# Kernel tuning notes

Hardware: AMD Instinct MI355X
Metric: run time of the kernel (lower is better)

## Reference

```python
import jax, jax.numpy as jnp
import numpy as np

VX, VY = 0.2, 0.2
X_OFF = VX / 2 + 0.0      # pc_range x_min = 0
Y_OFF = VY / 2 + (-40.0)  # pc_range y_min = -40
BN_EPS = 1e-3


def setup_inputs() -> dict:
    key = jax.random.key(0)
    k1, k2, k3, k4, k5, k6 = jax.random.split(key, 6)
    K, P, C_IN, C_AUG, C_OUT = 20000, 100, 4, 9, 64
    features = jax.random.normal(k1, (K, P, C_IN), dtype=jnp.float32)
    # at least 1 point per pillar (avoids div-by-zero, as in real voxelization)
    num_voxels = jax.random.randint(k2, (K,), 1, P + 1, dtype=jnp.int64)
    coors = jax.random.randint(k3, (K, 4), 0, 352, dtype=jnp.int64)
    W = jax.random.normal(k4, (C_AUG, C_OUT), dtype=jnp.float32) * (1.0 / np.sqrt(C_AUG))
    gamma = jnp.ones((C_OUT,), dtype=jnp.float32) + 0.1 * jax.random.normal(k5, (C_OUT,), dtype=jnp.float32)
    beta = 0.1 * jax.random.normal(k6, (C_OUT,), dtype=jnp.float32)
    return {"features": features, "num_voxels": num_voxels, "coors": coors,
            "W": W, "gamma": gamma, "beta": beta}


def reference(features, num_voxels, coors, W, gamma, beta):
    K, P, _ = features.shape
    dt = features.dtype
    pn = num_voxels.astype(dt)[:, None, None]                      # [K,1,1]
    cx = coors[:, 3].astype(dt)[:, None] * VX + X_OFF              # [K,1]
    cy = coors[:, 2].astype(dt)[:, None] * VY + Y_OFF              # [K,1]
    mask = (jnp.arange(P)[None, :] < num_voxels[:, None]).astype(dt)[..., None]  # [K,P,1]
    # cluster offset: point xyz minus per-pillar mean
    points_mean = features[..., :3].sum(axis=-2, keepdims=True) / pn
    f_cluster = features[..., :3] - points_mean                    # [K,P,3]
    # center offset: point xy minus pillar center
    f_center = jnp.stack([features[..., 0] - cx, features[..., 1] - cy], axis=-1)  # [K,P,2]
    feats = jnp.concatenate([features, f_cluster, f_center], axis=-1) * mask       # [K,P,9]
    # PFNLayer: Linear(no bias) -> BatchNorm1d (training-mode batch stats) -> ReLU -> max over points
    x = jnp.einsum('kpc,cu->kpu', feats, W)                        # [K,P,64]
    mu = x.mean(axis=(0, 1))
    var = ((x - mu) ** 2).mean(axis=(0, 1))
    x = (x - mu) * jax.lax.rsqrt(var + BN_EPS) * gamma + beta
    x = jax.nn.relu(x)
    return x.max(axis=1)                                           # [K,64] (squeezed)
```

## Files before the change

kernel.cpp:

```cpp
#include <hip/hip_runtime.h>


typedef float f32x2 __attribute__((ext_vector_type(2)));

#define NQ 14
#define NO 54
#define NP 68

__device__ __forceinline__ float wred(float v) {
#pragma unroll
  for (int off = 1; off < 64; off <<= 1) v += __shfl_xor(v, off, 64);
  return v;
}

__global__ void __launch_bounds__(512) pfn_main(
    const float4* __restrict__ feat, const int* __restrict__ nvox,
    const int* __restrict__ coors, const float* __restrict__ W, int K, int P,
    int nwaves, int nblocks, float* __restrict__ partials,
    float4* __restrict__ ext) {
  __shared__ float4 pts[8][102];
  __shared__ float redQ[8][NQ];
  __shared__ float redO[8][NO];
  const int lane = threadIdx.x & 63;
  const int wid = threadIdx.x >> 6;
  const int hl = lane & 31;
  const int p0 = lane >> 5;

  int c_i = lane, c2_i = lane;
  if (lane >= 9 && lane < NO) {
    int r = lane - 9, c = 0;
    while (r >= 9 - c) { r -= 9 - c; ++c; }
    c_i = c; c2_i = c + r;
  }
  const int gc = (c_i < 4) ? c_i : (c_i < 7 ? c_i - 4 : c_i - 7);
  const int gc2 = (c2_i < 4) ? c2_i : (c2_i < 7 ? c2_i - 4 : c2_i - 7);

  const f32x2* W2 = (const f32x2*)W;
  const f32x2 w4 = W2[4 * 32 + hl], w5 = W2[5 * 32 + hl];
  const f32x2 w6 = W2[6 * 32 + hl], w7 = W2[7 * 32 + hl];
  const f32x2 w8 = W2[8 * 32 + hl];
  const f32x2 wx = W2[0 * 32 + hl] + w4 + w7;
  const f32x2 wy = W2[1 * 32 + hl] + w5 + w8;
  const f32x2 wz = W2[2 * 32 + hl] + w6;
  const f32x2 w3 = W2[3 * 32 + hl];

  float gvx = 0, gvy = 0, gvz = 0, gvw = 0;
  float qxx = 0, qxy = 0, qxz = 0, qxw = 0, qyy = 0;
  float qyz = 0, qyw = 0, qzz = 0, qzw = 0, qww = 0;
  float oacc = 0;

  const int gw = (blockIdx.x * blockDim.x + threadIdx.x) >> 6;
  for (int k = gw; k < K; k += nwaves) {
    const size_t base = (size_t)k * P;
    const int nv = nvox[k];
    float sax = 0, say = 0, saz = 0;
    float svx = 0, svy = 0, svz = 0, svw = 0;
    for (int p = lane; p < P; p += 64) {
      float4 f = feat[base + p];
      pts[wid][p] = f;
      sax += f.x; say += f.y; saz += f.z;
      if (p < nv) {
        svx += f.x; svy += f.y; svz += f.z; svw += f.w;
        qxx = fmaf(f.x, f.x, qxx); qxy = fmaf(f.x, f.y, qxy);
        qxz = fmaf(f.x, f.z, qxz); qxw = fmaf(f.x, f.w, qxw);
        qyy = fmaf(f.y, f.y, qyy); qyz = fmaf(f.y, f.z, qyz);
        qyw = fmaf(f.y, f.w, qyw); qzz = fmaf(f.z, f.z, qzz);
        qzw = fmaf(f.z, f.w, qzw); qww = fmaf(f.w, f.w, qww);
      }
    }
    if ((nv & 1) && nv < P && lane == 0) pts[wid][nv] = pts[wid][0];
    const float rsax = wred(sax), rsay = wred(say), rsaz = wred(saz);
    const float rsvx = wred(svx), rsvy = wred(svy);
    const float rsvz = wred(svz), rsvw = wred(svw);
    gvx += svx; gvy += svy; gvz += svz; gvw += svw;

    const float nvf = (float)nv, inv = 1.f / nvf;
    const float mx = rsax * inv, my = rsay * inv, mz = rsaz * inv;
    const float cx = (float)coors[k * 4 + 3] * 0.2f + 0.1f;
    const float cy = (float)coors[k * 4 + 2] * 0.2f - 39.9f;

    if (lane < 9) {
      const float oc = (lane == 4) ? -mx : (lane == 5) ? -my
                     : (lane == 6) ? -mz : (lane == 7) ? -cx
                     : (lane == 8) ? -cy : 0.f;
      oacc = fmaf(nvf, oc, oacc);
    } else if (lane < NO) {
      const float oc = (c_i == 4) ? -mx : (c_i == 5) ? -my
                     : (c_i == 6) ? -mz : (c_i == 7) ? -cx
                     : (c_i == 8) ? -cy : 0.f;
      const float oc2 = (c2_i == 4) ? -mx : (c2_i == 5) ? -my
                      : (c2_i == 6) ? -mz : (c2_i == 7) ? -cx
                      : (c2_i == 8) ? -cy : 0.f;
      const float sgc = (gc == 0) ? rsvx : (gc == 1) ? rsvy
                      : (gc == 2) ? rsvz : rsvw;
      const float sgc2 = (gc2 == 0) ? rsvx : (gc2 == 1) ? rsvy
                       : (gc2 == 2) ? rsvz : rsvw;
      oacc += oc * sgc2 + oc2 * sgc + nvf * oc * oc2;
    }

    const f32x2 bias = -(mx * w4 + my * w5 + mz * w6 + cx * w7 + cy * w8);
    f32x2 bm0 = {-3e38f, -3e38f}, bm1 = {-3e38f, -3e38f};
    f32x2 bn0 = {3e38f, 3e38f}, bn1 = {3e38f, 3e38f};
    const int nvv = nv + (nv & 1);
    int p = 0;
    for (; p + 4 <= nvv; p += 4) {
      float4 fa = pts[wid][p + p0];
      float4 fb = pts[wid][p + 2 + p0];
      f32x2 ba = wx * fa.x + wy * fa.y + wz * fa.z + w3 * fa.w;
      f32x2 bb = wx * fb.x + wy * fb.y + wz * fb.z + w3 * fb.w;
      bm0.x = fmaxf(bm0.x, ba.x); bm0.y = fmaxf(bm0.y, ba.y);
      bn0.x = fminf(bn0.x, ba.x); bn0.y = fminf(bn0.y, ba.y);
      bm1.x = fmaxf(bm1.x, bb.x); bm1.y = fmaxf(bm1.y, bb.y);
      bn1.x = fminf(bn1.x, bb.x); bn1.y = fminf(bn1.y, bb.y);
    }
    for (; p < nvv; p += 2) {
      float4 fa = pts[wid][p + p0];
      f32x2 ba = wx * fa.x + wy * fa.y + wz * fa.z + w3 * fa.w;
      bm0.x = fmaxf(bm0.x, ba.x); bm0.y = fmaxf(bm0.y, ba.y);
      bn0.x = fminf(bn0.x, ba.x); bn0.y = fminf(bn0.y, ba.y);
    }
    f32x2 bm, bn;
    bm.x = fmaxf(bm0.x, bm1.x); bm.y = fmaxf(bm0.y, bm1.y);
    bn.x = fminf(bn0.x, bn1.x); bn.y = fminf(bn0.y, bn1.y);
    bm.x = fmaxf(bm.x, __shfl_xor(bm.x, 32, 64));
    bm.y = fmaxf(bm.y, __shfl_xor(bm.y, 32, 64));
    bn.x = fminf(bn.x, __shfl_xor(bn.x, 32, 64));
    bn.y = fminf(bn.y, __shfl_xor(bn.y, 32, 64));
    f32x2 vmax = bm + bias, vmin = bn + bias;
    if (nv < P) {
      vmax.x = fmaxf(vmax.x, 0.f); vmax.y = fmaxf(vmax.y, 0.f);
      vmin.x = fminf(vmin.x, 0.f); vmin.y = fminf(vmin.y, 0.f);
    }
    if (lane < 32) {
      float4 e; e.x = vmax.x; e.y = vmax.y; e.z = vmin.x; e.w = vmin.y;
      ext[(size_t)k * 32 + hl] = e;
    }
  }

  float qa[NQ] = {gvx, gvy, gvz, gvw, qxx, qxy, qxz,
                  qxw, qyy, qyz, qyw, qzz, qzw, qww};
#pragma unroll
  for (int i = 0; i < NQ; ++i) qa[i] = wred(qa[i]);
  if (lane == 0) {
#pragma unroll
    for (int i = 0; i < NQ; ++i) redQ[wid][i] = qa[i];
  }
  if (lane < NO) redO[wid][lane] = oacc;
  __syncthreads();
  const int t = threadIdx.x;
  if (t < NQ) {
    float s = 0;
#pragma unroll
    for (int w = 0; w < 8; ++w) s += redQ[w][t];
    partials[t * nblocks + blockIdx.x] = s;
  }
  if (t >= 64 && t < 64 + NO) {
    const int m = t - 64;
    float s = 0;
#pragma unroll
    for (int w = 0; w < 8; ++w) s += redO[w][m];
    partials[(NQ + m) * nblocks + blockIdx.x] = s;
  }
}

__global__ void __launch_bounds__(512) pfn_finalize(
    const float* __restrict__ partials, int nblocks,
    const float* __restrict__ W, const float* __restrict__ gamma,
    const float* __restrict__ beta, float invN, float* __restrict__ ss) {
  __shared__ float msum[NP];
  __shared__ float m54[NO];
  const int t = threadIdx.x;
  const int m = t >> 2, j = t & 3;
  if (m < NP) {
    const int chunk = nblocks >> 2;
    const float* row = partials + m * nblocks + j * chunk;
    float a0 = 0, a1 = 0, a2 = 0, a3 = 0, a4 = 0, a5 = 0, a6 = 0, a7 = 0;
    int b = 0;
    for (; b + 8 <= chunk; b += 8) {
      a0 += row[b];     a1 += row[b + 1]; a2 += row[b + 2]; a3 += row[b + 3];
      a4 += row[b + 4]; a5 += row[b + 5]; a6 += row[b + 6]; a7 += row[b + 7];
    }
    for (; b < chunk; ++b) a0 += row[b];
    float s = ((a0 + a1) + (a2 + a3)) + ((a4 + a5) + (a6 + a7));
    s += __shfl_xor(s, 1, 64);
    s += __shfl_xor(s, 2, 64);
    if (j == 0) msum[m] = s;
  }
  __syncthreads();
  if (t < NO) {
    float v;
    if (t < 9) {
      const int g = (t < 4) ? t : (t < 7 ? t - 4 : t - 7);
      v = msum[g] + msum[NQ + t];
    } else {
      int r = t - 9, c = 0;
      while (r >= 9 - c) { r -= 9 - c; ++c; }
      const int c2 = c + r;
      const int a = (c < 4) ? c : (c < 7 ? c - 4 : c - 7);
      const int b2 = (c2 < 4) ? c2 : (c2 < 7 ? c2 - 4 : c2 - 7);
      const int lo = a < b2 ? a : b2, hi = a < b2 ? b2 : a;
      const int qi = lo * (9 - lo) / 2 + (hi - lo);
      v = msum[4 + qi] + msum[NQ + t];
    }
    m54[t] = v;
  }
  __syncthreads();
  if (t < 64) {
    float wc[9];
#pragma unroll
    for (int c = 0; c < 9; ++c) wc[c] = W[c * 64 + t];
    float mu = 0.f;
#pragma unroll
    for (int c = 0; c < 9; ++c) mu += m54[c] * invN * wc[c];
    float ex2 = 0.f;
    int idx = 9;
#pragma unroll
    for (int c = 0; c < 9; ++c)
#pragma unroll
      for (int c2 = c; c2 < 9; ++c2) {
        float v = m54[idx] * invN * wc[c] * wc[c2];
        ex2 += (c == c2) ? v : 2.f * v;
        ++idx;
      }
    const float var = ex2 - mu * mu;
    const float scale = gamma[t] * rsqrtf(var + 1e-3f);
    ss[t] = scale;
    ss[64 + t] = beta[t] - mu * scale;
  }
}

__global__ void __launch_bounds__(256) pfn_apply(
    const float4* __restrict__ ext, const float* __restrict__ ss, int n,
    f32x2* __restrict__ out) {
  const int t = blockIdx.x * 256 + threadIdx.x;
  if (t >= n) return;
  const int l = t & 31;
  const float4 e = ext[t];
  const f32x2 sc = ((const f32x2*)ss)[l];
  const f32x2 sh = ((const f32x2*)(ss + 64))[l];
  const float v0 = (sc.x >= 0.f) ? e.x : e.z;
  const float v1 = (sc.y >= 0.f) ? e.y : e.w;
  f32x2 o;
  o.x = fmaxf(fmaf(sc.x, v0, sh.x), 0.f);
  o.y = fmaxf(fmaf(sc.y, v1, sh.y), 0.f);
  out[t] = o;
}

extern "C" void kernel_launch(void* const* d_in, const int* in_sizes, int n_in,
                              void* d_out, int out_size, void* d_ws,
                              size_t ws_size, hipStream_t stream) {
  const float4* feat = (const float4*)d_in[0];
  const int* nvox = (const int*)d_in[1];
  const int* coors = (const int*)d_in[2];
  const float* W = (const float*)d_in[3];
  const float* gamma = (const float*)d_in[4];
  const float* beta = (const float*)d_in[5];
  float* out = (float*)d_out;

  const int K = in_sizes[1];
  const int P = in_sizes[0] / (K * 4);

  float* ss = (float*)d_ws;
  float* partials = ss + 128;
  const int nblk = 512;
  float4* ext = (float4*)(partials + NP * nblk);

  pfn_main<<<nblk, 512, 0, stream>>>(feat, nvox, coors, W, K, P, nblk * 8,
                                     nblk, partials, ext);
  pfn_finalize<<<1, 512, 0, stream>>>(partials, nblk, W, gamma, beta,
                                      1.0f / (float)((long long)K * P), ss);
  const int n3 = K * 32;
  pfn_apply<<<(n3 + 255) / 256, 256, 0, stream>>>(ext, ss, n3, (f32x2*)out);
}
```

Before: 46.76 us.

## Prefetch next pillar into double-buffered LDS and restructure moment accumulation

Each wave now handles a contiguous run of pillars instead of striding across the grid. It prefetches the next pillar's features, voxel count and coordinates into registers while computing the current one, and double-buffers the shared-memory point tile. Per-pillar wave reductions of the valid-point sums are removed. Cross terms are instead kept as per-lane outer-product accumulators (S, u1, u2) and reduced once at the end, with the finalize kernel rebuilding the 54 second-moment entries from them. This cuts shuffle work and hides global load latency, at the cost of more registers and a contiguous assignment that may load-balance worse.

New measurement: 53.28 us. 14.0% more time.

```diff
diff --git a/kernel.cpp b/kernel.cpp
--- a/kernel.cpp
+++ b/kernel.cpp
@@ -3,175 +3,211 @@
 
 typedef float f32x2 __attribute__((ext_vector_type(2)));
 
-#define NQ 14
-#define NO 54
-#define NP 68
-
-__device__ __forceinline__ float wred(float v) {
+#define NR 54
+
+__device__ __forceinline__ float wred_add(float v) {
 #pragma unroll
   for (int off = 1; off < 64; off <<= 1) v += __shfl_xor(v, off, 64);
   return v;
+}
+__device__ __forceinline__ f32x2 pmax2(f32x2 a, f32x2 b) {
+  f32x2 r; r.x = fmaxf(a.x, b.x); r.y = fmaxf(a.y, b.y); return r;
+}
+__device__ __forceinline__ f32x2 pmin2(f32x2 a, f32x2 b) {
+  f32x2 r; r.x = fminf(a.x, b.x); r.y = fminf(a.y, b.y); return r;
 }
 
 __global__ void __launch_bounds__(512) pfn_main(
     const float4* __restrict__ feat, const int* __restrict__ nvox,
     const int* __restrict__ coors, const float* __restrict__ W, int K, int P,
-    int nwaves, int nblocks, float* __restrict__ partials,
+    int cnt, int nblocks, float* __restrict__ partials,
     float4* __restrict__ ext) {
-  __shared__ float4 pts[8][102];
-  __shared__ float redQ[8][NQ];
-  __shared__ float redO[8][NO];
+  __shared__ float4 pts[8][2][104];
+  __shared__ float red[8][NR];
   const int lane = threadIdx.x & 63;
   const int wid = threadIdx.x >> 6;
   const int hl = lane & 31;
   const int p0 = lane >> 5;
 
-  int c_i = lane, c2_i = lane;
-  if (lane >= 9 && lane < NO) {
-    int r = lane - 9, c = 0;
-    while (r >= 9 - c) { r -= 9 - c; ++c; }
-    c_i = c; c2_i = c + r;
-  }
-  const int gc = (c_i < 4) ? c_i : (c_i < 7 ? c_i - 4 : c_i - 7);
-  const int gc2 = (c2_i < 4) ? c2_i : (c2_i < 7 ? c2_i - 4 : c2_i - 7);
-
   const f32x2* W2 = (const f32x2*)W;
-  const f32x2 w4 = W2[4 * 32 + hl], w5 = W2[5 * 32 + hl];
-  const f32x2 w6 = W2[6 * 32 + hl], w7 = W2[7 * 32 + hl];
-  const f32x2 w8 = W2[8 * 32 + hl];
-  const f32x2 wx = W2[0 * 32 + hl] + w4 + w7;
-  const f32x2 wy = W2[1 * 32 + hl] + w5 + w8;
-  const f32x2 wz = W2[2 * 32 + hl] + w6;
+  const f32x2 v4 = W2[4 * 32 + hl], v5 = W2[5 * 32 + hl];
+  const f32x2 v6 = W2[6 * 32 + hl], v7 = W2[7 * 32 + hl];
+  const f32x2 v8 = W2[8 * 32 + hl];
+  const f32x2 wx = W2[0 * 32 + hl] + v4 + v7;
+  const f32x2 wy = W2[1 * 32 + hl] + v5 + v8;
+  const f32x2 wz = W2[2 * 32 + hl] + v6;
   const f32x2 w3 = W2[3 * 32 + hl];
 
-  float gvx = 0, gvy = 0, gvz = 0, gvw = 0;
-  float qxx = 0, qxy = 0, qxz = 0, qxw = 0, qyy = 0;
-  float qyz = 0, qyw = 0, qzz = 0, qzw = 0, qww = 0;
-  float oacc = 0;
-
-  const int gw = (blockIdx.x * blockDim.x + threadIdx.x) >> 6;
-  for (int k = gw; k < K; k += nwaves) {
-    const size_t base = (size_t)k * P;
-    const int nv = nvox[k];
-    float sax = 0, say = 0, saz = 0;
-    float svx = 0, svy = 0, svz = 0, svw = 0;
-    for (int p = lane; p < P; p += 64) {
-      float4 f = feat[base + p];
-      pts[wid][p] = f;
-      sax += f.x; say += f.y; saz += f.z;
-      if (p < nv) {
-        svx += f.x; svy += f.y; svz += f.z; svw += f.w;
-        qxx = fmaf(f.x, f.x, qxx); qxy = fmaf(f.x, f.y, qxy);
-        qxz = fmaf(f.x, f.z, qxz); qxw = fmaf(f.x, f.w, qxw);
-        qyy = fmaf(f.y, f.y, qyy); qyz = fmaf(f.y, f.z, qyz);
-        qyw = fmaf(f.y, f.w, qyw); qzz = fmaf(f.z, f.z, qzz);
-        qzw = fmaf(f.z, f.w, qzw); qww = fmaf(f.w, f.w, qww);
-      }
+  float q1[4] = {0, 0, 0, 0};
+  float q2[10] = {0, 0, 0, 0, 0, 0, 0, 0, 0, 0};
+  float S[20];
+  float u1[5] = {0, 0, 0, 0, 0};
+  float u2[15];
+#pragma unroll
+  for (int i = 0; i < 20; ++i) S[i] = 0.f;
+#pragma unroll
+  for (int i = 0; i < 15; ++i) u2[i] = 0.f;
+
+  const int gw = blockIdx.x * 8 + wid;
+  const int k0 = gw * cnt;
+  const int kend = (k0 + cnt < K) ? k0 + cnt : K;
+
+  if (k0 < kend) {
+    const bool hih = (64 + lane) < P;
+    size_t base = (size_t)k0 * P;
+    float4 f0 = feat[base + lane];
+    float4 f1;
+    if (hih) f1 = feat[base + 64 + lane];
+    int nv = nvox[k0];
+    float fcx = (float)coors[k0 * 4 + 3], fcy = (float)coors[k0 * 4 + 2];
+    int cur = 0;
+    for (int k = k0; k < kend; ++k) {
+      pts[wid][cur][lane] = f0;
+      if (hih) pts[wid][cur][64 + lane] = f1;
+      if ((nv & 1) && lane == 0) pts[wid][cur][nv] = f0;
+
+      float sax = f0.x, say = f0.y, saz = f0.z;
+      float svx = 0, svy = 0, svz = 0, svw = 0;
+      if (lane < nv) {
+        svx = f0.x; svy = f0.y; svz = f0.z; svw = f0.w;
+        q2[0] = fmaf(f0.x, f0.x, q2[0]); q2[1] = fmaf(f0.x, f0.y, q2[1]);
+        q2[2] = fmaf(f0.x, f0.z, q2[2]); q2[3] = fmaf(f0.x, f0.w, q2[3]);
+        q2[4] = fmaf(f0.y, f0.y, q2[4]); q2[5] = fmaf(f0.y, f0.z, q2[5]);
+        q2[6] = fmaf(f0.y, f0.w, q2[6]); q2[7] = fmaf(f0.z, f0.z, q2[7]);
+        q2[8] = fmaf(f0.z, f0.w, q2[8]); q2[9] = fmaf(f0.w, f0.w, q2[9]);
+      }
+      if (hih) {
+        sax += f1.x; say += f1.y; saz += f1.z;
+        if (64 + lane < nv) {
+          svx += f1.x; svy += f1.y; svz += f1.z; svw += f1.w;
+          q2[0] = fmaf(f1.x, f1.x, q2[0]); q2[1] = fmaf(f1.x, f1.y, q2[1]);
+          q2[2] = fmaf(f1.x, f1.z, q2[2]); q2[3] = fmaf(f1.x, f1.w, q2[3]);
+          q2[4] = fmaf(f1.y, f1.y, q2[4]); q2[5] = fmaf(f1.y, f1.z, q2[5]);
+          q2[6] = fmaf(f1.y, f1.w, q2[6]); q2[7] = fmaf(f1.z, f1.z, q2[7]);
+          q2[8] = fmaf(f1.z, f1.w, q2[8]); q2[9] = fmaf(f1.w, f1.w, q2[9]);
+        }
+      }
+
+      float4 f0n, f1n;
+      int nvn = nv;
+      float fcxn = fcx, fcyn = fcy;
+      if (k + 1 < kend) {
+        size_t nb = (size_t)(k + 1) * P;
+        f0n = feat[nb + lane];
+        if (hih) f1n = feat[nb + 64 + lane];
+        nvn = nvox[k + 1];
+        fcxn = (float)coors[(k + 1) * 4 + 3];
+        fcyn = (float)coors[(k + 1) * 4 + 2];
+      }
+
+      float rx = sax, ry = say, rz = saz;
+#pragma unroll
+      for (int off = 1; off < 64; off <<= 1) {
+        rx += __shfl_xor(rx, off, 64);
+        ry += __shfl_xor(ry, off, 64);
+        rz += __shfl_xor(rz, off, 64);
+      }
+      const float nvf = (float)nv, inv = 1.f / nvf;
+      const float cx = fcx * 0.2f + 0.1f, cy = fcy * 0.2f - 39.9f;
+      const float o0 = -rx * inv, o1 = -ry * inv, o2 = -rz * inv;
+      const float o3 = -cx, o4 = -cy;
+
+      const int nvv = nv + (nv & 1);
+      f32x2 bm0 = {-3e38f, -3e38f}, bm1 = {-3e38f, -3e38f};
+      f32x2 bn0 = {3e38f, 3e38f}, bn1 = {3e38f, 3e38f};
+      int p = 0;
+      for (; p + 4 <= nvv; p += 4) {
+        float4 fa = pts[wid][cur][p + p0];
+        float4 fb = pts[wid][cur][p + 2 + p0];
+        f32x2 ba = wx * fa.x + wy * fa.y + wz * fa.z + w3 * fa.w;
+        f32x2 bb = wx * fb.x + wy * fb.y + wz * fb.z + w3 * fb.w;
+        bm0 = pmax2(bm0, ba); bn0 = pmin2(bn0, ba);
+        bm1 = pmax2(bm1, bb); bn1 = pmin2(bn1, bb);
+      }
+      if (p < nvv) {
+        float4 fa = pts[wid][cur][p + p0];
+        f32x2 ba = wx * fa.x + wy * fa.y + wz * fa.z + w3 * fa.w;
+        bm0 = pmax2(bm0, ba); bn0 = pmin2(bn0, ba);
+      }
+      f32x2 bm = pmax2(bm0, bm1), bn = pmin2(bn0, bn1);
+      f32x2 tsw;
+      tsw.x = __shfl_xor(bm.x, 32, 64); tsw.y = __shfl_xor(bm.y, 32, 64);
+      bm = pmax2(bm, tsw);
+      tsw.x = __shfl_xor(bn.x, 32, 64); tsw.y = __shfl_xor(bn.y, 32, 64);
+      bn = pmin2(bn, tsw);
+      const f32x2 bias = v4 * o0 + v5 * o1 + v6 * o2 + v7 * o3 + v8 * o4;
+      f32x2 vmax = bm + bias, vmin = bn + bias;
+      if (nv < P) {
+        vmax.x = fmaxf(vmax.x, 0.f); vmax.y = fmaxf(vmax.y, 0.f);
+        vmin.x = fminf(vmin.x, 0.f); vmin.y = fminf(vmin.y, 0.f);
+      }
+      if (lane < 32) {
+        float4 e; e.x = vmax.x; e.y = vmax.y; e.z = vmin.x; e.w = vmin.y;
+        ext[(size_t)k * 32 + hl] = e;
+      }
+
+      q1[0] += svx; q1[1] += svy; q1[2] += svz; q1[3] += svw;
+      const float ov[5] = {o0, o1, o2, o3, o4};
+      const float sv[4] = {svx, svy, svz, svw};
+#pragma unroll
+      for (int a = 0; a < 4; ++a)
+#pragma unroll
+        for (int b = 0; b < 5; ++b)
+          S[a * 5 + b] = fmaf(sv[a], ov[b], S[a * 5 + b]);
+      float no[5];
+#pragma unroll
+      for (int b = 0; b < 5; ++b) { no[b] = nvf * ov[b]; u1[b] += no[b]; }
+      int ui = 0;
+#pragma unroll
+      for (int b = 0; b < 5; ++b)
+#pragma unroll
+        for (int b2 = b; b2 < 5; ++b2) {
+          u2[ui] = fmaf(no[b], ov[b2], u2[ui]);
+          ++ui;
+        }
+
+      f0 = f0n; f1 = f1n; nv = nvn; fcx = fcxn; fcy = fcyn; cur ^= 1;
     }
-    if ((nv & 1) && nv < P && lane == 0) pts[wid][nv] = pts[wid][0];
-    const float rsax = wred(sax), rsay = wred(say), rsaz = wred(saz);
-    const float rsvx = wred(svx), rsvy = wred(svy);
-    const float rsvz = wred(svz), rsvw = wred(svw);
-    gvx += svx; gvy += svy; gvz += svz; gvw += svw;
-
-    const float nvf = (float)nv, inv = 1.f / nvf;
-    const float mx = rsax * inv, my = rsay * inv, mz = rsaz * inv;
-    const float cx = (float)coors[k * 4 + 3] * 0.2f + 0.1f;
-    const float cy = (float)coors[k * 4 + 2] * 0.2f - 39.9f;
-
-    if (lane < 9) {
-      const float oc = (lane == 4) ? -mx : (lane == 5) ? -my
-                     : (lane == 6) ? -mz : (lane == 7) ? -cx
-                     : (lane == 8) ? -cy : 0.f;
-      oacc = fmaf(nvf, oc, oacc);
-    } else if (lane < NO) {
-      const float oc = (c_i == 4) ? -mx : (c_i == 5) ? -my
-                     : (c_i == 6) ? -mz : (c_i == 7) ? -cx
-                     : (c_i == 8) ? -cy : 0.f;
-      const float oc2 = (c2_i == 4) ? -mx : (c2_i == 5) ? -my
-                      : (c2_i == 6) ? -mz : (c2_i == 7) ? -cx
-                      : (c2_i == 8) ? -cy : 0.f;
-      const float sgc = (gc == 0) ? rsvx : (gc == 1) ? rsvy
-                      : (gc == 2) ? rsvz : rsvw;
-      const float sgc2 = (gc2 == 0) ? rsvx : (gc2 == 1) ? rsvy
-                       : (gc2 == 2) ? rsvz : rsvw;
-      oacc += oc * sgc2 + oc2 * sgc + nvf * oc * oc2;
+  }
+
+  {
+    float a34[34];
+#pragma unroll
+    for (int i = 0; i < 4; ++i) a34[i] = q1[i];
+#pragma unroll
+    for (int i = 0; i < 10; ++i) a34[4 + i] = q2[i];
+#pragma unroll
+    for (int i = 0; i < 20; ++i) a34[14 + i] = S[i];
+#pragma unroll
+    for (int i = 0; i < 34; ++i) a34[i] = wred_add(a34[i]);
+    if (lane == 0) {
+#pragma unroll
+      for (int i = 0; i < 34; ++i) red[wid][i] = a34[i];
+#pragma unroll
+      for (int j = 0; j < 5; ++j) red[wid][34 + j] = u1[j];
+#pragma unroll
+      for (int j = 0; j < 15; ++j) red[wid][39 + j] = u2[j];
     }
-
-    const f32x2 bias = -(mx * w4 + my * w5 + mz * w6 + cx * w7 + cy * w8);
-    f32x2 bm0 = {-3e38f, -3e38f}, bm1 = {-3e38f, -3e38f};
-    f32x2 bn0 = {3e38f, 3e38f}, bn1 = {3e38f, 3e38f};
-    const int nvv = nv + (nv & 1);
-    int p = 0;
-    for (; p + 4 <= nvv; p += 4) {
-      float4 fa = pts[wid][p + p0];
-      float4 fb = pts[wid][p + 2 + p0];
-      f32x2 ba = wx * fa.x + wy * fa.y + wz * fa.z + w3 * fa.w;
-      f32x2 bb = wx * fb.x + wy * fb.y + wz * fb.z + w3 * fb.w;
-      bm0.x = fmaxf(bm0.x, ba.x); bm0.y = fmaxf(bm0.y, ba.y);
-      bn0.x = fminf(bn0.x, ba.x); bn0.y = fminf(bn0.y, ba.y);
-      bm1.x = fmaxf(bm1.x, bb.x); bm1.y = fmaxf(bm1.y, bb.y);
-      bn1.x = fminf(bn1.x, bb.x); bn1.y = fminf(bn1.y, bb.y);
-    }
-    for (; p < nvv; p += 2) {
-      float4 fa = pts[wid][p + p0];
-      f32x2 ba = wx * fa.x + wy * fa.y + wz * fa.z + w3 * fa.w;
-      bm0.x = fmaxf(bm0.x, ba.x); bm0.y = fmaxf(bm0.y, ba.y);
-      bn0.x = fminf(bn0.x, ba.x); bn0.y = fminf(bn0.y, ba.y);
-    }
-    f32x2 bm, bn;
-    bm.x = fmaxf(bm0.x, bm1.x); bm.y = fmaxf(bm0.y, bm1.y);
-    bn.x = fminf(bn0.x, bn1.x); bn.y = fminf(bn0.y, bn1.y);
-    bm.x = fmaxf(bm.x, __shfl_xor(bm.x, 32, 64));
-    bm.y = fmaxf(bm.y, __shfl_xor(bm.y, 32, 64));
-    bn.x = fminf(bn.x, __shfl_xor(bn.x, 32, 64));
-    bn.y = fminf(bn.y, __shfl_xor(bn.y, 32, 64));
-    f32x2 vmax = bm + bias, vmin = bn + bias;
-    if (nv < P) {
-      vmax.x = fmaxf(vmax.x, 0.f); vmax.y = fmaxf(vmax.y, 0.f);
-      vmin.x = fminf(vmin.x, 0.f); vmin.y = fminf(vmin.y, 0.f);
-    }
-    if (lane < 32) {
-      float4 e; e.x = vmax.x; e.y = vmax.y; e.z = vmin.x; e.w = vmin.y;
-      ext[(size_t)k * 32 + hl] = e;
-    }
-  }
-
-  float qa[NQ] = {gvx, gvy, gvz, gvw, qxx, qxy, qxz,
-                  qxw, qyy, qyz, qyw, qzz, qzw, qww};
-#pragma unroll
-  for (int i = 0; i < NQ; ++i) qa[i] = wred(qa[i]);
-  if (lane == 0) {
-#pragma unroll
-    for (int i = 0; i < NQ; ++i) redQ[wid][i] = qa[i];
-  }
-  if (lane < NO) redO[wid][lane] = oacc;
+  }
   __syncthreads();
   const int t = threadIdx.x;
-  if (t < NQ) {
-    float s = 0;
-#pragma unroll
-    for (int w = 0; w < 8; ++w) s += redQ[w][t];
+  if (t < NR) {
+    float s = 0.f;
+#pragma unroll
+    for (int w = 0; w < 8; ++w) s += red[w][t];
     partials[t * nblocks + blockIdx.x] = s;
   }
-  if (t >= 64 && t < 64 + NO) {
-    const int m = t - 64;
-    float s = 0;
-#pragma unroll
-    for (int w = 0; w < 8; ++w) s += redO[w][m];
-    partials[(NQ + m) * nblocks + blockIdx.x] = s;
-  }
-}
-
-__global__ void __launch_bounds__(512) pfn_finalize(
+}
+
+__global__ void __launch_bounds__(256) pfn_finalize(
     const float* __restrict__ partials, int nblocks,
     const float* __restrict__ W, const float* __restrict__ gamma,
     const float* __restrict__ beta, float invN, float* __restrict__ ss) {
-  __shared__ float msum[NP];
-  __shared__ float m54[NO];
+  __shared__ float msum[NR];
+  __shared__ float m54[54];
   const int t = threadIdx.x;
   const int m = t >> 2, j = t & 3;
-  if (m < NP) {
+  if (m < NR) {
     const int chunk = nblocks >> 2;
     const float* row = partials + m * nblocks + j * chunk;
     float a0 = 0, a1 = 0, a2 = 0, a3 = 0, a4 = 0, a5 = 0, a6 = 0, a7 = 0;
@@ -187,11 +223,12 @@
     if (j == 0) msum[m] = s;
   }
   __syncthreads();
-  if (t < NO) {
+  if (t < 54) {
     float v;
     if (t < 9) {
       const int g = (t < 4) ? t : (t < 7 ? t - 4 : t - 7);
-      v = msum[g] + msum[NQ + t];
+      v = msum[g];
+      if (t >= 4) v += msum[34 + (t - 4)];
     } else {
       int r = t - 9, c = 0;
       while (r >= 9 - c) { r -= 9 - c; ++c; }
@@ -199,8 +236,13 @@
       const int a = (c < 4) ? c : (c < 7 ? c - 4 : c - 7);
       const int b2 = (c2 < 4) ? c2 : (c2 < 7 ? c2 - 4 : c2 - 7);
       const int lo = a < b2 ? a : b2, hi = a < b2 ? b2 : a;
-      const int qi = lo * (9 - lo) / 2 + (hi - lo);
-      v = msum[4 + qi] + msum[NQ + t];
+      v = msum[4 + lo * (9 - lo) / 2 + (hi - lo)];
+      if (c2 >= 4) v += msum[14 + a * 5 + (c2 - 4)];
+      if (c >= 4) v += msum[14 + b2 * 5 + (c - 4)];
+      if (c >= 4 && c2 >= 4) {
+        const int ua = c - 4, ub = c2 - 4;
+        v += msum[39 + ua * 5 - ua * (ua - 1) / 2 + (ub - ua)];
+      }
     }
     m54[t] = v;
   }
@@ -263,11 +305,14 @@
   float* ss = (float*)d_ws;
   float* partials = ss + 128;
   const int nblk = 512;
-  float4* ext = (float4*)(partials + NP * nblk);
-
-  pfn_main<<<nblk, 512, 0, stream>>>(feat, nvox, coors, W, K, P, nblk * 8,
-                                     nblk, partials, ext);
-  pfn_finalize<<<1, 512, 0, stream>>>(partials, nblk, W, gamma, beta,
+  float4* ext = (float4*)(partials + NR * nblk);
+
+  const int nwaves = nblk * 8;
+  const int cnt = (K + nwaves - 1) / nwaves;
+
+  pfn_main<<<nblk, 512, 0, stream>>>(feat, nvox, coors, W, K, P, cnt, nblk,
+                                     partials, ext);
+  pfn_finalize<<<1, 256, 0, stream>>>(partials, nblk, W, gamma, beta,
                                       1.0f / (float)((long long)K * P), ss);
   const int n3 = K * 32;
   pfn_apply<<<(n3 + 255) / 256, 256, 0, stream>>>(ext, ss, n3, (f32x2*)out);
```
